# Performance work log

Hardware: AMD Instinct MI355X
Metric: run time of the kernel (lower is better)

## Reference

```python
import jax, jax.numpy as jnp
import numpy as np

S_DIM = 8      # state_dim
O_DIM = 4      # obs_dim
HID = (S_DIM * S_DIM + O_DIM * O_DIM) * 10   # 800
BATCH = 128
SEQ = 32
NS = 16        # num_samples
P_DROP = 0.2
DROP_KEY = jax.random.key(42)

def f_dyn(x):
    # synthetic nonlinear dynamics (stand-in for system_model.f, vmapped over batch)
    return 0.9 * x + 0.1 * jnp.sin(x)

def h_obs(x):
    # synthetic nonlinear observation (stand-in for system_model.h)
    return jnp.tanh(x[..., :O_DIM])

def l2_normalize(x, eps=1e-12):
    # matches torch F.normalize(p=2, dim=1): x / max(||x||, eps)
    n = jnp.linalg.norm(x, axis=-1, keepdims=True)
    return x / jnp.maximum(n, eps)

def setup_inputs() -> dict:
    key = jax.random.key(0)
    ks = jax.random.split(key, 8)
    g = 0.02
    return {
        "y_seq": jax.random.normal(ks[0], (BATCH, SEQ, O_DIM), dtype=jnp.float32),
        "W1": jax.random.normal(ks[1], (HID, S_DIM + O_DIM), dtype=jnp.float32) * g,
        "b1": jnp.zeros((HID,), jnp.float32),
        "W_ih": jax.random.normal(ks[2], (3 * HID, HID), dtype=jnp.float32) * g,
        "W_hh": jax.random.normal(ks[3], (3 * HID, HID), dtype=jnp.float32) * g,
        "b_ih": jnp.zeros((3 * HID,), jnp.float32),
        "b_hh": jnp.zeros((3 * HID,), jnp.float32),
        "W_out": jax.random.normal(ks[4], (S_DIM * O_DIM, HID), dtype=jnp.float32) * g,
        "b_out": jnp.zeros((S_DIM * O_DIM,), jnp.float32),
        "num_samples": NS,
    }

def _forward(y_seq, W1, b1, W_ih, W_hh, b_ih, b_hh, W_out, b_out, num_samples):
    B = y_seq.shape[0]
    keep = 1.0 - P_DROP

    def gru_cell(x, h):
        # torch nn.GRU single-step math; x,h: [..., HID]
        gi = x @ W_ih.T + b_ih
        gh = h @ W_hh.T + b_hh
        gi_r, gi_z, gi_n = jnp.split(gi, 3, axis=-1)
        gh_r, gh_z, gh_n = jnp.split(gh, 3, axis=-1)
        r = jax.nn.sigmoid(gi_r + gh_r)
        z = jax.nn.sigmoid(gi_z + gh_z)
        n = jnp.tanh(gi_n + r * gh_n)
        return (1.0 - z) * n + z * h

    def step(carry, inp):
        x_prev, dx_prev, h_ens = carry            # [B,S], [B,S], [NS,B,HID]
        y_t, t = inp
        x_pred = f_dyn(x_prev)                    # [B,S] (same for every sample j)
        y_hat = h_obs(x_pred)                     # [B,O]
        innov = y_t - y_hat                       # [B,O]
        nn_in = jnp.concatenate([l2_normalize(dx_prev), l2_normalize(innov)], axis=-1)
        a = jax.nn.relu(nn_in @ W1.T + b1)        # [B,HID]
        k1, k2 = jax.random.split(jax.random.fold_in(DROP_KEY, t))
        m1 = jax.random.bernoulli(k1, keep, (num_samples, B, HID)).astype(a.dtype)
        a_ens = a[None] * m1 / keep               # MC-dropout per ensemble member
        h_new = gru_cell(a_ens, h_ens)            # [NS,B,HID] (vectorized over samples)
        K_vec = h_new @ W_out.T + b_out           # [NS,B,S*O]
        m2 = jax.random.bernoulli(k2, keep, K_vec.shape).astype(a.dtype)
        K = (K_vec * m2 / keep).reshape(num_samples, B, S_DIM, O_DIM)
        ens = x_pred[None] + jnp.einsum('jbso,bo->jbs', K, innov)  # [NS,B,S]
        x_filt = ens.mean(axis=0)                 # [B,S]
        diff = ens - x_filt[None]                 # [NS,B,S]
        P_filt = jnp.einsum('jbs,jbt->bst', diff, diff) / num_samples
        dx = x_filt - x_pred                      # delta_x_prev = x_filt - f(x_prev)
        return (x_filt, dx, h_new), (x_filt, P_filt)

    x0 = jnp.zeros((B, S_DIM), y_seq.dtype)
    dx0 = jnp.zeros((B, S_DIM), y_seq.dtype)
    h0 = jnp.zeros((num_samples, B, HID), y_seq.dtype)
    ts = jnp.arange(y_seq.shape[1])
    _, (xs, Ps) = jax.lax.scan(step, (x0, dx0, h0), (jnp.swapaxes(y_seq, 0, 1), ts))
    # xs: [T,B,S] -> [B,T,S]; Ps: [T,B,S,S] -> [B,T,S,S]
    return jnp.swapaxes(xs, 0, 1), jnp.swapaxes(Ps, 0, 1)

def reference(y_seq, W1, b1, W_ih, W_hh, b_ih, b_hh, W_out, b_out, num_samples):
    return _forward(y_seq, W1, b1, W_ih, W_hh, b_ih, b_hh, W_out, b_out, num_samples)
```

## Files before the change

### kernel.cpp

```cpp
#include <hip/hip_runtime.h>
#include <stdint.h>

#define NSAMP 16
#define BATCH 128
#define SEQLEN 32
#define SDIM 8
#define ODIM 4
#define HID 800
#define MROWS (NSAMP * BATCH)
#define KEEPP 0.8f

typedef __attribute__((ext_vector_type(8))) short short8v;
typedef __attribute__((ext_vector_type(4))) float float4v;

__host__ __device__ __forceinline__ void tf2x32(uint32_t k0, uint32_t k1,
                                                uint32_t x0, uint32_t x1,
                                                uint32_t& o0, uint32_t& o1) {
  uint32_t ks2 = k0 ^ k1 ^ 0x1BD11BDAu;
  x0 += k0; x1 += k1;
#define TFR(r) { x0 += x1; x1 = (x1 << (r)) | (x1 >> (32 - (r))); x1 ^= x0; }
  TFR(13) TFR(15) TFR(26) TFR(6)
  x0 += k1; x1 += ks2 + 1u;
  TFR(17) TFR(29) TFR(16) TFR(24)
  x0 += ks2; x1 += k0 + 2u;
  TFR(13) TFR(15) TFR(26) TFR(6)
  x0 += k0; x1 += k1 + 3u;
  TFR(17) TFR(29) TFR(16) TFR(24)
  x0 += k1; x1 += ks2 + 4u;
  TFR(13) TFR(15) TFR(26) TFR(6)
  x0 += ks2; x1 += k0 + 5u;
#undef TFR
  o0 = x0; o1 = x1;
}

__device__ __forceinline__ float bits_to_unit(uint32_t bits) {
  return __uint_as_float((bits >> 9) | 0x3F800000u) - 1.0f;
}

__device__ __forceinline__ float tf_uniform_part(uint32_t k0, uint32_t k1, uint32_t idx) {
  uint32_t b1, b2;
  tf2x32(k0, k1, 0u, idx, b1, b2);
  return bits_to_unit(b1 ^ b2);
}

__device__ __forceinline__ ushort f2bf(float f) {
  uint32_t u = __float_as_uint(f);
  uint32_t r = (u + 0x7FFFu + ((u >> 16) & 1u)) >> 16;
  return (ushort)r;
}

__device__ __forceinline__ void bar_sync() {
  __builtin_amdgcn_sched_barrier(0);
  __builtin_amdgcn_s_barrier();
  __builtin_amdgcn_sched_barrier(0);
}

__global__ void convert_w_kernel(const float* __restrict__ W_ih, const float* __restrict__ W_hh,
                                 ushort* __restrict__ Wib, ushort* __restrict__ Whb) {
  int i = (blockIdx.x * 256 + threadIdx.x) * 4;
  if (i >= 2400 * HID) return;
  float4 v1 = *reinterpret_cast<const float4*>(W_ih + i);
  float4 v2 = *reinterpret_cast<const float4*>(W_hh + i);
  ushort4 o1, o2;
  o1.x = f2bf(v1.x); o1.y = f2bf(v1.y); o1.z = f2bf(v1.z); o1.w = f2bf(v1.w);
  o2.x = f2bf(v2.x); o2.y = f2bf(v2.y); o2.z = f2bf(v2.z); o2.w = f2bf(v2.w);
  *reinterpret_cast<ushort4*>(Wib + i) = o1;
  *reinterpret_cast<ushort4*>(Whb + i) = o2;
}

__global__ void transpose_wout_kernel(const float* __restrict__ W_out, float* __restrict__ WoutT) {
  int i = blockIdx.x * 256 + threadIdx.x;
  if (i < 32 * HID) {
    int o = i / HID, k = i - o * HID;
    WoutT[k * 32 + o] = W_out[i];
  }
}

__global__ void a_ens_kernel(const float* __restrict__ a, ushort* __restrict__ aeb,
                             uint32_t k0, uint32_t k1) {
  int base = (blockIdx.x * blockDim.x + threadIdx.x) * 4;
  if (base >= MROWS * HID) return;
  int row = base / HID;
  int b = row % BATCH;
  int col = base - row * HID;
  float4 av = *reinterpret_cast<const float4*>(a + b * HID + col);
  ushort4 ov;
#pragma unroll
  for (int q = 0; q < 4; ++q) {
    float u = tf_uniform_part(k0, k1, (uint32_t)(base + q));
    float f = (&av.x)[q] * ((u < KEEPP) ? 1.25f : 0.0f);
    (&ov.x)[q] = f2bf(f);
  }
  *reinterpret_cast<ushort4*>(aeb + base) = ov;
}

#define LDSB 12288

__global__ __launch_bounds__(256, 2) void gru_mfma_kernel(
    const ushort* __restrict__ aeb, const ushort* __restrict__ hb,
    const ushort* __restrict__ Wib, const ushort* __restrict__ Whb,
    const float* __restrict__ h_old,
    const float* __restrict__ b_ih, const float* __restrict__ b_hh,
    float* __restrict__ h_new, ushort* __restrict__ h_new_b) {
  __shared__ __align__(1024) char lds[2 * LDSB];

  const int tid = threadIdx.x;
  const int wid = tid >> 6;
  const int lane = tid & 63;

  const int bid = blockIdx.x;
  const int xcd = bid & 7;
  const int q = bid >> 3;
  const int mm = q / 25;
  const int nblk = q - mm * 25;
  const int m0 = (xcd * 2 + mm) * 128;
  const int n0 = nblk * 32;

  float4v acc[6][2][2];
#pragma unroll
  for (int g = 0; g < 6; ++g)
#pragma unroll
    for (int mf = 0; mf < 2; ++mf)
#pragma unroll
      for (int nf = 0; nf < 2; ++nf)
        acc[g][mf][nf] = (float4v)(0.0f);

  const int rlo = lane >> 2;
  const int sslot = (lane & 3) ^ ((lane >> 3) & 3);
  const int kg = lane >> 4;
  const int l15 = lane & 15;

  const ushort* gp[3];
  int ldso[3];
#pragma unroll
  for (int s = 0; s < 3; ++s) {
    int i = s * 4 + wid;
    int g = i >> 1, half = i & 1;
    ldso[s] = g * 2048 + half * 1024;
    const ushort* base = (g < 3) ? Wib : Whb;
    int wrow = n0 + (g % 3) * HID + half * 16 + rlo;
    gp[s] = base + (size_t)wrow * HID + sslot * 8;
  }

  const ushort* ap[2][2];
#pragma unroll
  for (int mf = 0; mf < 2; ++mf) {
    const int row = m0 + wid * 32 + mf * 16 + l15;
    ap[0][mf] = aeb + (size_t)row * HID + kg * 8;
    ap[1][mf] = hb + (size_t)row * HID + kg * 8;
  }

  short8v ar0[2][2], ar1[2][2];

#define STAGE_B(BUF) do {                                                        \
    _Pragma("unroll")                                                            \
    for (int s = 0; s < 3; ++s) {                                                \
      __builtin_amdgcn_global_load_lds(                                          \
          (const __attribute__((address_space(1))) void*)gp[s],                  \
          (__attribute__((address_space(3))) void*)(lds + (BUF)*LDSB + ldso[s]), \
          16, 0, 0);                                                             \
      gp[s] += 32;                                                               \
    }                                                                            \
  } while (0)

#define LOAD_A(SET) do {                                                         \
    _Pragma("unroll")                                                            \
    for (int s2 = 0; s2 < 2; ++s2)                                               \
      _Pragma("unroll")                                                          \
      for (int mf = 0; mf < 2; ++mf) {                                           \
        SET[s2][mf] = *reinterpret_cast<const short8v*>(ap[s2][mf]);             \
        ap[s2][mf] += 32;                                                        \
      }                                                                          \
  } while (0)

#define COMPUTE(BUF, SET) do {                                                   \
    const char* lb = lds + (BUF)*LDSB;                                           \
    short8v bfr[6][2];                                                           \
    _Pragma("unroll")                                                            \
    for (int g = 0; g < 6; ++g)                                                  \
      _Pragma("unroll")                                                          \
      for (int nf = 0; nf < 2; ++nf) {                                           \
        int row = nf * 16 + l15;                                                 \
        int off = g * 2048 + row * 64 + ((kg ^ ((row >> 1) & 3)) << 4);          \
        bfr[g][nf] = *reinterpret_cast<const short8v*>(lb + off);                \
      }                                                                          \
    _Pragma("unroll")                                                            \
    for (int g = 0; g < 6; ++g) {                                                \
      const int src = (g < 3) ? 0 : 1;                                           \
      _Pragma("unroll")                                                          \
      for (int mf = 0; mf < 2; ++mf)                                             \
        _Pragma("unroll")                                                        \
        for (int nf = 0; nf < 2; ++nf)                                           \
          acc[g][mf][nf] = __builtin_amdgcn_mfma_f32_16x16x32_bf16(              \
              SET[src][mf], bfr[g][nf], acc[g][mf][nf], 0, 0, 0);                \
    }                                                                            \
  } while (0)

  STAGE_B(0);
  LOAD_A(ar0);
#pragma unroll 1
  for (int k = 0; k < 24; k += 2) {
    STAGE_B(1);
    LOAD_A(ar1);
    asm volatile("s_waitcnt vmcnt(7)" ::: "memory");
    bar_sync();
    COMPUTE(0, ar0);
    bar_sync();
    STAGE_B(0);
    LOAD_A(ar0);
    asm volatile("s_waitcnt vmcnt(7)" ::: "memory");
    bar_sync();
    COMPUTE(1, ar1);
    bar_sync();
  }
  asm volatile("s_waitcnt vmcnt(0)" ::: "memory");
  bar_sync();
  COMPUTE(0, ar0);

  const int rowq = (lane >> 4) * 4;
#pragma unroll
  for (int nf = 0; nf < 2; ++nf) {
    const int col = n0 + nf * 16 + l15;
    const float bir = b_ih[col], biz = b_ih[col + HID], bin = b_ih[col + 2 * HID];
    const float bhr = b_hh[col], bhz = b_hh[col + HID], bhn = b_hh[col + 2 * HID];
#pragma unroll
    for (int mf = 0; mf < 2; ++mf) {
#pragma unroll
      for (int reg = 0; reg < 4; ++reg) {
        const int m = m0 + wid * 32 + mf * 16 + rowq + reg;
        float gir = acc[0][mf][nf][reg] + bir;
        float giz = acc[1][mf][nf][reg] + biz;
        float gin = acc[2][mf][nf][reg] + bin;
        float ghr = acc[3][mf][nf][reg] + bhr;
        float ghz = acc[4][mf][nf][reg] + bhz;
        float ghn = acc[5][mf][nf][reg] + bhn;
        float r = 1.0f / (1.0f + expf(-(gir + ghr)));
        float z = 1.0f / (1.0f + expf(-(giz + ghz)));
        float nval = tanhf(gin + r * ghn);
        float hv = h_old[(size_t)m * HID + col];
        float res = (1.0f - z) * nval + z * hv;
        h_new[(size_t)m * HID + col] = res;
        h_new_b[(size_t)m * HID + col] = f2bf(res);
      }
    }
  }
#undef STAGE_B
#undef LOAD_A
#undef COMPUTE
}

__global__ void kvec_ens_kernel(const float* __restrict__ h_new,
                                const float* __restrict__ WoutT,
                                const float* __restrict__ b_out,
                                const float* __restrict__ x_pred,
                                const float* __restrict__ innov,
                                float* __restrict__ ens,
                                uint32_t k0, uint32_t k1) {
  const int jb = blockIdx.x;
  const int b = jb & (BATCH - 1);
  const int tid = threadIdx.x;
  const int o = tid & 31;
  const int kk = tid >> 5;

  const float* hrow = h_new + (size_t)jb * HID;
  float partial = 0.0f;
  for (int k = kk * 100; k < kk * 100 + 100; ++k)
    partial = fmaf(hrow[k], WoutT[k * 32 + o], partial);

  __shared__ float red[8][32];
  __shared__ float Kv[32];
  red[kk][o] = partial;
  __syncthreads();
  if (tid < 32) {
    float s = 0.0f;
#pragma unroll
    for (int q = 0; q < 8; ++q) s += red[q][tid];
    s += b_out[tid];
    float u = tf_uniform_part(k0, k1, (uint32_t)(jb * 32 + tid));
    Kv[tid] = (u < KEEPP) ? s * 1.25f : 0.0f;
  }
  __syncthreads();
  if (tid < SDIM) {
    float s = x_pred[b * SDIM + tid];
#pragma unroll
    for (int oo = 0; oo < ODIM; ++oo)
      s = fmaf(Kv[tid * ODIM + oo], innov[b * ODIM + oo], s);
    ens[jb * SDIM + tid] = s;
  }
}

__global__ void reduce_prep_kernel(const float* __restrict__ ens,
                                   float* __restrict__ x_pred,
                                   float* __restrict__ innov,
                                   const float* __restrict__ y_seq,
                                   const float* __restrict__ W1,
                                   const float* __restrict__ b1,
                                   float* __restrict__ a,
                                   float* __restrict__ out_xs, float* __restrict__ out_Ps,
                                   int t) {
  const int b = blockIdx.x;
  const int tid = threadIdx.x;
  __shared__ float e[NSAMP][SDIM];
  __shared__ float xf[SDIM];
  __shared__ float dxs[SDIM];
  __shared__ float xpn[SDIM];
  __shared__ float inv[ODIM];
  __shared__ float nin[SDIM + ODIM];

  if (t >= 0) {
    if (tid < NSAMP * SDIM) {
      int j = tid >> 3, s = tid & 7;
      e[j][s] = ens[(j * BATCH + b) * SDIM + s];
    }
    __syncthreads();
    if (tid < SDIM) {
      float s = 0.0f;
#pragma unroll
      for (int j = 0; j < NSAMP; ++j) s += e[j][tid];
      s *= (1.0f / NSAMP);
      xf[tid] = s;
      out_xs[(b * SEQLEN + t) * SDIM + tid] = s;
      dxs[tid] = s - x_pred[b * SDIM + tid];
    }
    __syncthreads();
    if (tid < SDIM * SDIM) {
      int s = tid >> 3, u = tid & 7;
      float accv = 0.0f;
#pragma unroll
      for (int j = 0; j < NSAMP; ++j)
        accv += (e[j][s] - xf[s]) * (e[j][u] - xf[u]);
      out_Ps[((b * SEQLEN + t) * SDIM + s) * SDIM + u] = accv * (1.0f / NSAMP);
    }
  } else {
    if (tid < SDIM) { xf[tid] = 0.0f; dxs[tid] = 0.0f; }
  }
  if (t == SEQLEN - 1) return;
  __syncthreads();
  if (tid < SDIM) {
    float x = xf[tid];
    float xp = 0.9f * x + 0.1f * sinf(x);
    xpn[tid] = xp;
    x_pred[b * SDIM + tid] = xp;
  }
  __syncthreads();
  if (tid < ODIM) {
    float yh = tanhf(xpn[tid]);
    float iv = y_seq[(b * SEQLEN + (t + 1)) * ODIM + tid] - yh;
    inv[tid] = iv;
    innov[b * ODIM + tid] = iv;
  }
  __syncthreads();
  if (tid == 0) {
    float nd = 0.0f;
    for (int s = 0; s < SDIM; ++s) nd += dxs[s] * dxs[s];
    nd = fmaxf(sqrtf(nd), 1e-12f);
    for (int s = 0; s < SDIM; ++s) nin[s] = dxs[s] / nd;
    float ni = 0.0f;
    for (int o2 = 0; o2 < ODIM; ++o2) ni += inv[o2] * inv[o2];
    ni = fmaxf(sqrtf(ni), 1e-12f);
    for (int o2 = 0; o2 < ODIM; ++o2) nin[SDIM + o2] = inv[o2] / ni;
  }
  __syncthreads();
  for (int i = tid; i < HID; i += blockDim.x) {
    float s = b1[i];
#pragma unroll
    for (int c = 0; c < 12; ++c) s = fmaf(nin[c], W1[i * 12 + c], s);
    a[b * HID + i] = fmaxf(s, 0.0f);
  }
}

extern "C" void kernel_launch(void* const* d_in, const int* in_sizes, int n_in,
                              void* d_out, int out_size, void* d_ws, size_t ws_size,
                              hipStream_t stream) {
  (void)in_sizes; (void)n_in; (void)out_size; (void)ws_size;
  const float* y_seq = (const float*)d_in[0];
  const float* W1 = (const float*)d_in[1];
  const float* b1 = (const float*)d_in[2];
  const float* W_ih = (const float*)d_in[3];
  const float* W_hh = (const float*)d_in[4];
  const float* b_ih = (const float*)d_in[5];
  const float* b_hh = (const float*)d_in[6];
  const float* W_out = (const float*)d_in[7];
  const float* b_out = (const float*)d_in[8];

  char* ws = (char*)d_ws;
  size_t off = 0;
  float* h_a = (float*)(ws + off);    off += (size_t)MROWS * HID * 4;
  float* h_b = (float*)(ws + off);    off += (size_t)MROWS * HID * 4;
  ushort* hb_a = (ushort*)(ws + off); off += (size_t)MROWS * HID * 2;
  ushort* hb_b = (ushort*)(ws + off); off += (size_t)MROWS * HID * 2;
  ushort* aeb = (ushort*)(ws + off);  off += (size_t)MROWS * HID * 2;
  ushort* Wib = (ushort*)(ws + off);  off += (size_t)2400 * HID * 2;
  ushort* Whb = (ushort*)(ws + off);  off += (size_t)2400 * HID * 2;
  float* a_buf = (float*)(ws + off);  off += (size_t)BATCH * HID * 4;
  float* WoutT = (float*)(ws + off);  off += (size_t)HID * 32 * 4;
  float* x_pred = (float*)(ws + off); off += (size_t)BATCH * SDIM * 4;
  float* innov = (float*)(ws + off);  off += (size_t)BATCH * ODIM * 4;
  float* ens = (float*)(ws + off);    off += (size_t)NSAMP * BATCH * SDIM * 4;

  float* out_xs = (float*)d_out;
  float* out_Ps = out_xs + (size_t)BATCH * SEQLEN * SDIM;

  hipMemsetAsync(h_a, 0, (size_t)MROWS * HID * 4, stream);
  hipMemsetAsync(hb_a, 0, (size_t)MROWS * HID * 2, stream);
  convert_w_kernel<<<1875, 256, 0, stream>>>(W_ih, W_hh, Wib, Whb);
  transpose_wout_kernel<<<100, 256, 0, stream>>>(W_out, WoutT);
  reduce_prep_kernel<<<BATCH, 256, 0, stream>>>(ens, x_pred, innov, y_seq, W1, b1,
                                                a_buf, out_xs, out_Ps, -1);

  float* hc = h_a;  float* hn = h_b;
  ushort* hcb = hb_a; ushort* hnb = hb_b;
  for (int t = 0; t < SEQLEN; ++t) {
    uint32_t kt0, kt1, k1a, k1b, k2a, k2b;
    tf2x32(0u, 42u, 0u, (uint32_t)t, kt0, kt1);
    tf2x32(kt0, kt1, 0u, 0u, k1a, k1b);
    tf2x32(kt0, kt1, 0u, 1u, k2a, k2b);

    a_ens_kernel<<<1600, 256, 0, stream>>>(a_buf, aeb, k1a, k1b);
    gru_mfma_kernel<<<400, 256, 0, stream>>>(aeb, hcb, Wib, Whb, hc, b_ih, b_hh, hn, hnb);
    kvec_ens_kernel<<<MROWS, 256, 0, stream>>>(hn, WoutT, b_out, x_pred, innov, ens, k2a, k2b);
    reduce_prep_kernel<<<BATCH, 256, 0, stream>>>(ens, x_pred, innov, y_seq, W1, b1,
                                                  a_buf, out_xs, out_Ps, t);
    float* tmp = hc; hc = hn; hn = tmp;
    ushort* tmpb = hcb; hcb = hnb; hnb = tmpb;
  }
}
```

Baseline: 2.087 ms.

## Deepen GRU GEMM LDS pipeline to four buffers and read bf16 hidden state in kvec

The GRU MFMA kernel moves from a two-buffer to a four-buffer LDS ring for the weight tiles. It prefetches two stages ahead, drops one barrier per iteration, and raises wave priority around the MFMA block. This is meant to hide more global load latency. The kvec kernel now reads the bf16 copy of the new hidden state instead of the fp32 one, which halves its activation traffic but lowers the precision of the output projection. The larger LDS footprint (48KB per block) may cut occupancy given the launch bounds of 2 blocks.

```diff
diff --git a/kernel.cpp b/kernel.cpp
--- a/kernel.cpp
+++ b/kernel.cpp
@@ -49,6 +49,10 @@
   return (ushort)r;
 }
 
+__device__ __forceinline__ float bf2f(ushort u) {
+  return __uint_as_float((uint32_t)u << 16);
+}
+
 __device__ __forceinline__ void bar_sync() {
   __builtin_amdgcn_sched_barrier(0);
   __builtin_amdgcn_s_barrier();
@@ -102,7 +106,7 @@
     const float* __restrict__ h_old,
     const float* __restrict__ b_ih, const float* __restrict__ b_hh,
     float* __restrict__ h_new, ushort* __restrict__ h_new_b) {
-  __shared__ __align__(1024) char lds[2 * LDSB];
+  __shared__ __align__(1024) char lds[4 * LDSB];
 
   const int tid = threadIdx.x;
   const int wid = tid >> 6;
@@ -152,12 +156,12 @@
 
   short8v ar0[2][2], ar1[2][2];
 
-#define STAGE_B(BUF) do {                                                        \
+#define STAGE_T(BUFI) do {                                                       \
     _Pragma("unroll")                                                            \
     for (int s = 0; s < 3; ++s) {                                                \
       __builtin_amdgcn_global_load_lds(                                          \
           (const __attribute__((address_space(1))) void*)gp[s],                  \
-          (__attribute__((address_space(3))) void*)(lds + (BUF)*LDSB + ldso[s]), \
+          (__attribute__((address_space(3))) void*)(lds + (BUFI)*LDSB + ldso[s]),\
           16, 0, 0);                                                             \
       gp[s] += 32;                                                               \
     }                                                                            \
@@ -173,8 +177,8 @@
       }                                                                          \
   } while (0)
 
-#define COMPUTE(BUF, SET) do {                                                   \
-    const char* lb = lds + (BUF)*LDSB;                                           \
+#define COMPUTE(BUFI, SET) do {                                                  \
+    const char* lb = lds + (BUFI)*LDSB;                                          \
     short8v bfr[6][2];                                                           \
     _Pragma("unroll")                                                            \
     for (int g = 0; g < 6; ++g)                                                  \
@@ -184,6 +188,7 @@
         int off = g * 2048 + row * 64 + ((kg ^ ((row >> 1) & 3)) << 4);          \
         bfr[g][nf] = *reinterpret_cast<const short8v*>(lb + off);                \
       }                                                                          \
+    __builtin_amdgcn_s_setprio(1);                                               \
     _Pragma("unroll")                                                            \
     for (int g = 0; g < 6; ++g) {                                                \
       const int src = (g < 3) ? 0 : 1;                                           \
@@ -194,25 +199,35 @@
           acc[g][mf][nf] = __builtin_amdgcn_mfma_f32_16x16x32_bf16(              \
               SET[src][mf], bfr[g][nf], acc[g][mf][nf], 0, 0, 0);                \
     }                                                                            \
+    __builtin_amdgcn_s_setprio(0);                                               \
   } while (0)
 
-  STAGE_B(0);
+  STAGE_T(0);
   LOAD_A(ar0);
+  STAGE_T(1);
+
 #pragma unroll 1
-  for (int k = 0; k < 24; k += 2) {
-    STAGE_B(1);
+  for (int p = 0; p < 22; p += 2) {
     LOAD_A(ar1);
-    asm volatile("s_waitcnt vmcnt(7)" ::: "memory");
+    STAGE_T((p + 2) & 3);
+    asm volatile("s_waitcnt vmcnt(10)" ::: "memory");
     bar_sync();
-    COMPUTE(0, ar0);
+    COMPUTE(p & 3, ar0);
+    LOAD_A(ar0);
+    STAGE_T((p + 3) & 3);
+    asm volatile("s_waitcnt vmcnt(10)" ::: "memory");
     bar_sync();
-    STAGE_B(0);
-    LOAD_A(ar0);
-    asm volatile("s_waitcnt vmcnt(7)" ::: "memory");
-    bar_sync();
-    COMPUTE(1, ar1);
-    bar_sync();
-  }
+    COMPUTE((p + 1) & 3, ar1);
+  }
+  LOAD_A(ar1);
+  STAGE_T(0);
+  asm volatile("s_waitcnt vmcnt(10)" ::: "memory");
+  bar_sync();
+  COMPUTE(2, ar0);
+  LOAD_A(ar0);
+  asm volatile("s_waitcnt vmcnt(7)" ::: "memory");
+  bar_sync();
+  COMPUTE(3, ar1);
   asm volatile("s_waitcnt vmcnt(0)" ::: "memory");
   bar_sync();
   COMPUTE(0, ar0);
@@ -244,12 +259,12 @@
       }
     }
   }
-#undef STAGE_B
+#undef STAGE_T
 #undef LOAD_A
 #undef COMPUTE
 }
 
-__global__ void kvec_ens_kernel(const float* __restrict__ h_new,
+__global__ void kvec_ens_kernel(const ushort* __restrict__ hnb,
                                 const float* __restrict__ WoutT,
                                 const float* __restrict__ b_out,
                                 const float* __restrict__ x_pred,
@@ -262,10 +277,11 @@
   const int o = tid & 31;
   const int kk = tid >> 5;
 
-  const float* hrow = h_new + (size_t)jb * HID;
+  const ushort* hrow = hnb + (size_t)jb * HID + kk * 100;
+  const float* wc = WoutT + kk * 100 * 32 + o;
   float partial = 0.0f;
-  for (int k = kk * 100; k < kk * 100 + 100; ++k)
-    partial = fmaf(hrow[k], WoutT[k * 32 + o], partial);
+  for (int k = 0; k < 100; ++k)
+    partial = fmaf(bf2f(hrow[k]), wc[k * 32], partial);
 
   __shared__ float red[8][32];
   __shared__ float Kv[32];
@@ -418,7 +434,7 @@
 
     a_ens_kernel<<<1600, 256, 0, stream>>>(a_buf, aeb, k1a, k1b);
     gru_mfma_kernel<<<400, 256, 0, stream>>>(aeb, hcb, Wib, Whb, hc, b_ih, b_hh, hn, hnb);
-    kvec_ens_kernel<<<MROWS, 256, 0, stream>>>(hn, WoutT, b_out, x_pred, innov, ens, k2a, k2b);
+    kvec_ens_kernel<<<MROWS, 256, 0, stream>>>(hnb, WoutT, b_out, x_pred, innov, ens, k2a, k2b);
     reduce_prep_kernel<<<BATCH, 256, 0, stream>>>(ens, x_pred, innov, y_seq, W1, b1,
                                                   a_buf, out_xs, out_Ps, t);
     float* tmp = hc; hc = hn; hn = tmp;
```

New measurement: 1.828 ms. 12.4% less time.

## Store activations and hidden state in MFMA fragment-tiled bf16 layout

Applied to the files above, without the earlier changes.

Replaces the row-major activation and hidden buffers with a fragment-tiled bf16 layout, so each wave's A-operand load is one contiguous 1KB chunk per k-step. The fp32 hidden-state copy is dropped: the GRU epilogue reads the previous state from bf16 and writes only bf16, and the K-vector kernel reads the tiled bf16 state. It also adds s_setprio around the MFMA block and remaps grid indices for XCD locality. The cost is extra rounding of the recurrent state to bf16 at every step, which can drift from the fp32 reference, plus scattered 2-byte stores in the epilogue.

```diff
diff --git a/kernel.cpp b/kernel.cpp
--- a/kernel.cpp
+++ b/kernel.cpp
@@ -9,6 +9,7 @@
 #define HID 800
 #define MROWS (NSAMP * BATCH)
 #define KEEPP 0.8f
+#define MTSTRIDE 12800
 
 typedef __attribute__((ext_vector_type(8))) short short8v;
 typedef __attribute__((ext_vector_type(4))) float float4v;
@@ -49,6 +50,10 @@
   return (ushort)r;
 }
 
+__device__ __forceinline__ float bf2f(ushort u) {
+  return __uint_as_float((uint32_t)u << 16);
+}
+
 __device__ __forceinline__ void bar_sync() {
   __builtin_amdgcn_sched_barrier(0);
   __builtin_amdgcn_s_barrier();
@@ -76,45 +81,51 @@
   }
 }
 
-__global__ void a_ens_kernel(const float* __restrict__ a, ushort* __restrict__ aeb,
+__global__ void a_ens_kernel(const float* __restrict__ a_buf, ushort* __restrict__ AF,
                              uint32_t k0, uint32_t k1) {
-  int base = (blockIdx.x * blockDim.x + threadIdx.x) * 4;
-  if (base >= MROWS * HID) return;
-  int row = base / HID;
-  int b = row % BATCH;
-  int col = base - row * HID;
-  float4 av = *reinterpret_cast<const float4*>(a + b * HID + col);
-  ushort4 ov;
-#pragma unroll
-  for (int q = 0; q < 4; ++q) {
-    float u = tf_uniform_part(k0, k1, (uint32_t)(base + q));
-    float f = (&av.x)[q] * ((u < KEEPP) ? 1.25f : 0.0f);
-    (&ov.x)[q] = f2bf(f);
-  }
-  *reinterpret_cast<ushort4*>(aeb + base) = ov;
-}
-
-#define LDSB 12288
+  const int bid = blockIdx.x;
+  const int panel = bid & 15;
+  const int q = bid >> 4;
+  const int w4 = q * 4 + (threadIdx.x >> 6);
+  const int lane = threadIdx.x & 63;
+  const int mt = panel * 8 + w4 / 25;
+  const int kt = w4 % 25;
+  const int row = mt * 16 + (lane & 15);
+  const int b = row & (BATCH - 1);
+  const int k = kt * 32 + (lane >> 4) * 8;
+  const float* src = a_buf + (size_t)b * HID + k;
+  float4 v0 = *reinterpret_cast<const float4*>(src);
+  float4 v1 = *reinterpret_cast<const float4*>(src + 4);
+  const uint32_t base = (uint32_t)(row * HID + k);
+  ushort o[8];
+#pragma unroll
+  for (int qq = 0; qq < 4; ++qq) {
+    float u = tf_uniform_part(k0, k1, base + qq);
+    o[qq] = f2bf((&v0.x)[qq] * ((u < KEEPP) ? 1.25f : 0.0f));
+  }
+#pragma unroll
+  for (int qq = 0; qq < 4; ++qq) {
+    float u = tf_uniform_part(k0, k1, base + 4 + qq);
+    o[4 + qq] = f2bf((&v1.x)[qq] * ((u < KEEPP) ? 1.25f : 0.0f));
+  }
+  *reinterpret_cast<short8v*>(AF + ((size_t)(mt * 25 + kt) * 64 + lane) * 8) =
+      *reinterpret_cast<const short8v*>(o);
+}
+
+#define LDSB2 12288
 
 __global__ __launch_bounds__(256, 2) void gru_mfma_kernel(
-    const ushort* __restrict__ aeb, const ushort* __restrict__ hb,
+    const ushort* __restrict__ AF, const ushort* __restrict__ HFi,
     const ushort* __restrict__ Wib, const ushort* __restrict__ Whb,
-    const float* __restrict__ h_old,
     const float* __restrict__ b_ih, const float* __restrict__ b_hh,
-    float* __restrict__ h_new, ushort* __restrict__ h_new_b) {
-  __shared__ __align__(1024) char lds[2 * LDSB];
-
+    ushort* __restrict__ HFo) {
+  __shared__ __align__(1024) char lds[2 * LDSB2];
   const int tid = threadIdx.x;
   const int wid = tid >> 6;
   const int lane = tid & 63;
-
-  const int bid = blockIdx.x;
-  const int xcd = bid & 7;
-  const int q = bid >> 3;
-  const int mm = q / 25;
-  const int nblk = q - mm * 25;
-  const int m0 = (xcd * 2 + mm) * 128;
-  const int n0 = nblk * 32;
+  const int bx = blockIdx.x;
+  const int by = blockIdx.y;
+  const int n0 = by * 32;
 
   float4v acc[6][2][2];
 #pragma unroll
@@ -145,36 +156,35 @@
   const ushort* ap[2][2];
 #pragma unroll
   for (int mf = 0; mf < 2; ++mf) {
-    const int row = m0 + wid * 32 + mf * 16 + l15;
-    ap[0][mf] = aeb + (size_t)row * HID + kg * 8;
-    ap[1][mf] = hb + (size_t)row * HID + kg * 8;
-  }
-
-  short8v ar0[2][2], ar1[2][2];
+    const size_t mt = (size_t)(bx * 8 + wid * 2 + mf);
+    ap[0][mf] = AF + mt * MTSTRIDE + (size_t)lane * 8;
+    ap[1][mf] = HFi + mt * MTSTRIDE + (size_t)lane * 8;
+  }
+  short8v s0v[2][2], s1v[2][2];
 
 #define STAGE_B(BUF) do {                                                        \
     _Pragma("unroll")                                                            \
     for (int s = 0; s < 3; ++s) {                                                \
       __builtin_amdgcn_global_load_lds(                                          \
           (const __attribute__((address_space(1))) void*)gp[s],                  \
-          (__attribute__((address_space(3))) void*)(lds + (BUF)*LDSB + ldso[s]), \
+          (__attribute__((address_space(3))) void*)(lds + (BUF)*LDSB2 + ldso[s]),\
           16, 0, 0);                                                             \
       gp[s] += 32;                                                               \
     }                                                                            \
   } while (0)
 
-#define LOAD_A(SET) do {                                                         \
+#define LOADA(SET) do {                                                          \
     _Pragma("unroll")                                                            \
-    for (int s2 = 0; s2 < 2; ++s2)                                               \
+    for (int sx = 0; sx < 2; ++sx)                                               \
       _Pragma("unroll")                                                          \
       for (int mf = 0; mf < 2; ++mf) {                                           \
-        SET[s2][mf] = *reinterpret_cast<const short8v*>(ap[s2][mf]);             \
-        ap[s2][mf] += 32;                                                        \
+        SET[sx][mf] = *reinterpret_cast<const short8v*>(ap[sx][mf]);             \
+        ap[sx][mf] += 512;                                                       \
       }                                                                          \
   } while (0)
 
 #define COMPUTE(BUF, SET) do {                                                   \
-    const char* lb = lds + (BUF)*LDSB;                                           \
+    const char* lb = lds + (BUF)*LDSB2;                                          \
     short8v bfr[6][2];                                                           \
     _Pragma("unroll")                                                            \
     for (int g = 0; g < 6; ++g)                                                  \
@@ -184,6 +194,7 @@
         int off = g * 2048 + row * 64 + ((kg ^ ((row >> 1) & 3)) << 4);          \
         bfr[g][nf] = *reinterpret_cast<const short8v*>(lb + off);                \
       }                                                                          \
+    __builtin_amdgcn_s_setprio(1);                                               \
     _Pragma("unroll")                                                            \
     for (int g = 0; g < 6; ++g) {                                                \
       const int src = (g < 3) ? 0 : 1;                                           \
@@ -194,78 +205,89 @@
           acc[g][mf][nf] = __builtin_amdgcn_mfma_f32_16x16x32_bf16(              \
               SET[src][mf], bfr[g][nf], acc[g][mf][nf], 0, 0, 0);                \
     }                                                                            \
+    __builtin_amdgcn_s_setprio(0);                                               \
   } while (0)
 
   STAGE_B(0);
-  LOAD_A(ar0);
+  LOADA(s0v);
 #pragma unroll 1
   for (int k = 0; k < 24; k += 2) {
     STAGE_B(1);
-    LOAD_A(ar1);
+    LOADA(s1v);
     asm volatile("s_waitcnt vmcnt(7)" ::: "memory");
     bar_sync();
-    COMPUTE(0, ar0);
+    COMPUTE(0, s0v);
     bar_sync();
     STAGE_B(0);
-    LOAD_A(ar0);
+    LOADA(s0v);
     asm volatile("s_waitcnt vmcnt(7)" ::: "memory");
     bar_sync();
-    COMPUTE(1, ar1);
+    COMPUTE(1, s1v);
     bar_sync();
   }
   asm volatile("s_waitcnt vmcnt(0)" ::: "memory");
   bar_sync();
-  COMPUTE(0, ar0);
+  COMPUTE(0, s0v);
 
   const int rowq = (lane >> 4) * 4;
 #pragma unroll
   for (int nf = 0; nf < 2; ++nf) {
     const int col = n0 + nf * 16 + l15;
+    const int klocal = nf * 16 + l15;
     const float bir = b_ih[col], biz = b_ih[col + HID], bin = b_ih[col + 2 * HID];
     const float bhr = b_hh[col], bhz = b_hh[col + HID], bhn = b_hh[col + 2 * HID];
 #pragma unroll
     for (int mf = 0; mf < 2; ++mf) {
 #pragma unroll
       for (int reg = 0; reg < 4; ++reg) {
-        const int m = m0 + wid * 32 + mf * 16 + rowq + reg;
+        const int r = wid * 32 + mf * 16 + rowq + reg;
+        const size_t mtr = (size_t)(bx * 8 + (r >> 4));
+        const size_t fo = (mtr * 25 + (size_t)by) * 512 +
+                          (size_t)((r & 15) + ((klocal >> 3) << 4)) * 8 + (klocal & 7);
         float gir = acc[0][mf][nf][reg] + bir;
         float giz = acc[1][mf][nf][reg] + biz;
         float gin = acc[2][mf][nf][reg] + bin;
         float ghr = acc[3][mf][nf][reg] + bhr;
         float ghz = acc[4][mf][nf][reg] + bhz;
         float ghn = acc[5][mf][nf][reg] + bhn;
-        float r = 1.0f / (1.0f + expf(-(gir + ghr)));
+        float rg = 1.0f / (1.0f + expf(-(gir + ghr)));
         float z = 1.0f / (1.0f + expf(-(giz + ghz)));
-        float nval = tanhf(gin + r * ghn);
-        float hv = h_old[(size_t)m * HID + col];
+        float nval = tanhf(gin + rg * ghn);
+        float hv = bf2f(HFi[fo]);
         float res = (1.0f - z) * nval + z * hv;
-        h_new[(size_t)m * HID + col] = res;
-        h_new_b[(size_t)m * HID + col] = f2bf(res);
+        HFo[fo] = f2bf(res);
       }
     }
   }
 #undef STAGE_B
-#undef LOAD_A
+#undef LOADA
 #undef COMPUTE
 }
 
-__global__ void kvec_ens_kernel(const float* __restrict__ h_new,
+__global__ void kvec_ens_kernel(const ushort* __restrict__ HF,
                                 const float* __restrict__ WoutT,
                                 const float* __restrict__ b_out,
                                 const float* __restrict__ x_pred,
                                 const float* __restrict__ innov,
                                 float* __restrict__ ens,
                                 uint32_t k0, uint32_t k1) {
-  const int jb = blockIdx.x;
+  const int bid = blockIdx.x;
+  const int x = bid & 7, i = bid >> 3;
+  const int jb = (x + (i >> 7) * 8) * 128 + (i & 127);
   const int b = jb & (BATCH - 1);
   const int tid = threadIdx.x;
   const int o = tid & 31;
   const int kk = tid >> 5;
 
-  const float* hrow = h_new + (size_t)jb * HID;
+  const ushort* hbase = HF + (size_t)(jb >> 4) * MTSTRIDE;
+  const int r15 = jb & 15;
   float partial = 0.0f;
-  for (int k = kk * 100; k < kk * 100 + 100; ++k)
-    partial = fmaf(hrow[k], WoutT[k * 32 + o], partial);
+  for (int q = 0; q < 100; ++q) {
+    int k = kk * 100 + q;
+    int kt = k >> 5, kl = k & 31;
+    float hvv = bf2f(hbase[(size_t)kt * 512 + (size_t)(r15 + ((kl >> 3) << 4)) * 8 + (kl & 7)]);
+    partial = fmaf(hvv, WoutT[k * 32 + o], partial);
+  }
 
   __shared__ float red[8][32];
   __shared__ float Kv[32];
@@ -385,11 +407,9 @@
 
   char* ws = (char*)d_ws;
   size_t off = 0;
-  float* h_a = (float*)(ws + off);    off += (size_t)MROWS * HID * 4;
-  float* h_b = (float*)(ws + off);    off += (size_t)MROWS * HID * 4;
-  ushort* hb_a = (ushort*)(ws + off); off += (size_t)MROWS * HID * 2;
-  ushort* hb_b = (ushort*)(ws + off); off += (size_t)MROWS * HID * 2;
-  ushort* aeb = (ushort*)(ws + off);  off += (size_t)MROWS * HID * 2;
+  ushort* hf_a = (ushort*)(ws + off); off += (size_t)MROWS * HID * 2;
+  ushort* hf_b = (ushort*)(ws + off); off += (size_t)MROWS * HID * 2;
+  ushort* AF = (ushort*)(ws + off);   off += (size_t)MROWS * HID * 2;
   ushort* Wib = (ushort*)(ws + off);  off += (size_t)2400 * HID * 2;
   ushort* Whb = (ushort*)(ws + off);  off += (size_t)2400 * HID * 2;
   float* a_buf = (float*)(ws + off);  off += (size_t)BATCH * HID * 4;
@@ -401,27 +421,25 @@
   float* out_xs = (float*)d_out;
   float* out_Ps = out_xs + (size_t)BATCH * SEQLEN * SDIM;
 
-  hipMemsetAsync(h_a, 0, (size_t)MROWS * HID * 4, stream);
-  hipMemsetAsync(hb_a, 0, (size_t)MROWS * HID * 2, stream);
+  hipMemsetAsync(hf_a, 0, (size_t)MROWS * HID * 2, stream);
   convert_w_kernel<<<1875, 256, 0, stream>>>(W_ih, W_hh, Wib, Whb);
   transpose_wout_kernel<<<100, 256, 0, stream>>>(W_out, WoutT);
   reduce_prep_kernel<<<BATCH, 256, 0, stream>>>(ens, x_pred, innov, y_seq, W1, b1,
                                                 a_buf, out_xs, out_Ps, -1);
 
-  float* hc = h_a;  float* hn = h_b;
-  ushort* hcb = hb_a; ushort* hnb = hb_b;
+  ushort* hfc = hf_a; ushort* hfn = hf_b;
+  dim3 gg(16, 25);
   for (int t = 0; t < SEQLEN; ++t) {
     uint32_t kt0, kt1, k1a, k1b, k2a, k2b;
     tf2x32(0u, 42u, 0u, (uint32_t)t, kt0, kt1);
     tf2x32(kt0, kt1, 0u, 0u, k1a, k1b);
     tf2x32(kt0, kt1, 0u, 1u, k2a, k2b);
 
-    a_ens_kernel<<<1600, 256, 0, stream>>>(a_buf, aeb, k1a, k1b);
-    gru_mfma_kernel<<<400, 256, 0, stream>>>(aeb, hcb, Wib, Whb, hc, b_ih, b_hh, hn, hnb);
-    kvec_ens_kernel<<<MROWS, 256, 0, stream>>>(hn, WoutT, b_out, x_pred, innov, ens, k2a, k2b);
+    a_ens_kernel<<<800, 256, 0, stream>>>(a_buf, AF, k1a, k1b);
+    gru_mfma_kernel<<<gg, 256, 0, stream>>>(AF, hfc, Wib, Whb, b_ih, b_hh, hfn);
+    kvec_ens_kernel<<<MROWS, 256, 0, stream>>>(hfn, WoutT, b_out, x_pred, innov, ens, k2a, k2b);
     reduce_prep_kernel<<<BATCH, 256, 0, stream>>>(ens, x_pred, innov, y_seq, W1, b1,
                                                   a_buf, out_xs, out_Ps, t);
-    float* tmp = hc; hc = hn; hn = tmp;
-    ushort* tmpb = hcb; hcb = hnb; hnb = tmpb;
-  }
-}
+    ushort* tmpf = hfc; hfc = hfn; hfn = tmpf;
+  }
+}
```

Measured after the change: 1.988 ms. 1.05x faster.
